# Kernel tuning notes

Hardware: AMD Instinct MI355X
Metric: run time of the kernel (lower is better)

The kernel has to match this reference:

```python
import math
import jax, jax.numpy as jnp
import numpy as np

B, S, D, L = 8, 4096, 1024, 16

def setup_inputs() -> dict:
    key = jax.random.key(0)
    k1, k2, k3 = jax.random.split(key, 3)
    memory = jax.random.normal(k1, (B, S, D), dtype=jnp.float32)
    summarizer = jax.random.normal(k2, (L, D), dtype=jnp.float32) * 0.02
    w_proj = jax.random.normal(k3, (1, L), dtype=jnp.float32) * (1.0 / math.sqrt(L))
    return {"memory": memory, "summarizer": summarizer, "w_proj": w_proj}

def reference(memory, summarizer, w_proj):
    # scores: [B, L, S] = summarizer @ memory^T / sqrt(D)
    d = summarizer.shape[-1]
    scores = jnp.einsum('ld,bsd->bls', summarizer, memory) / jnp.sqrt(jnp.asarray(d, memory.dtype))
    p_attn = jax.nn.softmax(scores, axis=-1)            # softmax over sequence S
    ctx = jnp.einsum('bls,bsd->bld', p_attn, memory)    # [B, L, D]
    # nn.Linear(L, 1, bias=False) applied to ctx.transpose(-1,-2): [B, D, L] @ W^T -> [B, D, 1]
    out = jnp.einsum('bld,l->bd', ctx, w_proj[0])       # [B, D]
    return out[:, None, :]                              # [B, 1, D] after final transpose
```

## Files before the change

### kernel.cpp

```cpp
#include <hip/hip_runtime.h>

#define SS 4096
#define DD 1024
#define LL 16

typedef __attribute__((ext_vector_type(8))) short short8;
typedef __attribute__((ext_vector_type(4))) float fl4;
typedef __attribute__((ext_vector_type(2))) float fl2;

static __device__ __forceinline__ short f2bf(float f) {
    unsigned u = __float_as_uint(f);
    u += 0x7FFFu + ((u >> 16) & 1u);
    return (short)(u >> 16);
}

static __device__ __forceinline__ short8 pack8(fl4 a, fl4 b) {
    short8 r;
    r[0] = f2bf(a[0]); r[1] = f2bf(a[1]); r[2] = f2bf(a[2]); r[3] = f2bf(a[3]);
    r[4] = f2bf(b[0]); r[5] = f2bf(b[1]); r[6] = f2bf(b[2]); r[7] = f2bf(b[3]);
    return r;
}

__global__ __launch_bounds__(512) void k_main(const float* __restrict__ mem,
                                              const float* __restrict__ summ,
                                              float* __restrict__ part,
                                              float* __restrict__ Zpart) {
    __shared__ float scr[2][8][256];
    __shared__ float e_lds[2][16][LL];

    int blk = blockIdx.x;
    int b   = blk >> 6;
    int s0  = (blk & 63) << 6;
    int t    = threadIdx.x;
    int wv   = t >> 6;
    int lane = t & 63;
    int o  = lane & 15;
    int qd = lane >> 4;

    short8 afr[4];
    {
        const float* arow = summ + o * DD + wv * 128 + qd * 8;
        #pragma unroll
        for (int j = 0; j < 4; ++j) {
            fl4 a0 = *(const fl4*)(arow + j * 32);
            fl4 a1 = *(const fl4*)(arow + j * 32 + 4);
            afr[j] = pack8(a0, a1);
        }
    }

    fl2 ctx[LL];
    #pragma unroll
    for (int l = 0; l < LL; ++l) ctx[l] = (fl2){0.f, 0.f};
    fl4 zacc = {0.f, 0.f, 0.f, 0.f};
    const float scale = 0.03125f;

    const float* gb = mem + ((size_t)b * SS + s0) * DD;

    #pragma unroll 2
    for (int c = 0; c < 4; ++c) {
        const float* brow = gb + (size_t)(c * 16 + o) * DD + wv * 128 + qd * 8;
        fl4 acc = {0.f, 0.f, 0.f, 0.f};
        #pragma unroll
        for (int j = 0; j < 4; ++j) {
            fl4 f0 = *(const fl4*)(brow + j * 32);
            fl4 f1 = *(const fl4*)(brow + j * 32 + 4);
            acc = __builtin_amdgcn_mfma_f32_16x16x32_bf16(afr[j], pack8(f0, f1),
                                                          acc, 0, 0, 0);
        }
        *(fl4*)&scr[c & 1][wv][lane * 4] = acc;
        asm volatile("s_waitcnt lgkmcnt(0)" ::: "memory");
        __builtin_amdgcn_s_barrier();
        __builtin_amdgcn_sched_barrier(0);

        if (wv == 0) {
            fl4 sum = {0.f, 0.f, 0.f, 0.f};
            #pragma unroll
            for (int w8 = 0; w8 < 8; ++w8)
                sum += *(const fl4*)&scr[c & 1][w8][lane * 4];
            fl4 ev;
            #pragma unroll
            for (int r = 0; r < 4; ++r) ev[r] = __expf(sum[r] * scale);
            *(fl4*)&e_lds[c & 1][o][qd * 4] = ev;
            zacc += ev;
        }
        asm volatile("s_waitcnt lgkmcnt(0)" ::: "memory");
        __builtin_amdgcn_s_barrier();
        __builtin_amdgcn_sched_barrier(0);

        const float* mrow = gb + (size_t)(c * 16) * DD + wv * 128 + lane * 2;
        #pragma unroll 4
        for (int s = 0; s < 16; ++s) {
            fl2 m2 = *(const fl2*)(mrow + (size_t)s * DD);
            #pragma unroll
            for (int g4 = 0; g4 < 4; ++g4) {
                fl4 e4 = *(const fl4*)&e_lds[c & 1][s][g4 * 4];
                ctx[g4 * 4 + 0] += e4[0] * m2;
                ctx[g4 * 4 + 1] += e4[1] * m2;
                ctx[g4 * 4 + 2] += e4[2] * m2;
                ctx[g4 * 4 + 3] += e4[3] * m2;
            }
        }
    }

    float* pp = part + (size_t)blk * LL * DD + wv * 128 + lane * 2;
    #pragma unroll
    for (int l = 0; l < LL; ++l) *(fl2*)(pp + (size_t)l * DD) = ctx[l];

    if (wv == 0) {
        #pragma unroll
        for (int r = 0; r < 4; ++r) {
            float v = zacc[r];
            v += __shfl_xor(v, 1, 64);
            v += __shfl_xor(v, 2, 64);
            v += __shfl_xor(v, 4, 64);
            v += __shfl_xor(v, 8, 64);
            zacc[r] = v;
        }
        if (o == 0) *(fl4*)&Zpart[blk * LL + qd * 4] = zacc;
    }
}

__global__ __launch_bounds__(256) void k_out(const float* __restrict__ part,
                                             const float* __restrict__ Zpart,
                                             const float* __restrict__ w,
                                             float* __restrict__ out) {
    int blkid = blockIdx.x;
    int b  = blkid >> 5;
    int d0 = (blkid & 31) << 5;
    int t = threadIdx.x;
    __shared__ float coef[LL];
    __shared__ fl4 red[32][8];

    if (t < LL) {
        float Z = 0.f;
        #pragma unroll
        for (int s = 0; s < 64; ++s) Z += Zpart[(b * 64 + s) * LL + t];
        coef[t] = w[t] / Z;
    }
    __syncthreads();

    int dq = t & 7;
    int sg = t >> 3;
    fl4 acc = {0.f, 0.f, 0.f, 0.f};
    #pragma unroll
    for (int h = 0; h < 2; ++h) {
        const float* pb = part + (size_t)(b * 64 + sg + h * 32) * LL * DD + d0 + dq * 4;
        #pragma unroll
        for (int l = 0; l < LL; ++l) {
            fl4 v = *(const fl4*)(pb + (size_t)l * DD);
            acc += coef[l] * v;
        }
    }
    red[sg][dq] = acc;
    __syncthreads();

    if (t < 8) {
        fl4 s = {0.f, 0.f, 0.f, 0.f};
        #pragma unroll
        for (int g = 0; g < 32; ++g) s += red[g][t];
        *(fl4*)&out[b * DD + d0 + t * 4] = s;
    }
}

extern "C" void kernel_launch(void* const* d_in, const int* in_sizes, int n_in,
                              void* d_out, int out_size, void* d_ws, size_t ws_size,
                              hipStream_t stream) {
    const float* mem  = (const float*)d_in[0];
    const float* summ = (const float*)d_in[1];
    const float* w    = (const float*)d_in[2];
    float* out = (float*)d_out;

    char* ws = (char*)d_ws;
    float* Zpart = (float*)ws;
    float* part  = (float*)(ws + 64 * 1024);

    k_main<<<512, 512, 0, stream>>>(mem, summ, part, Zpart);
    k_out<<<256, 256, 0, stream>>>(part, Zpart, w, out);
}
```

Baseline: 216.6 us.

## Compute full-D scores per wave to remove per-chunk cross-wave reductions

Result: slower. 221.7 us (+2.3%).

```diff
diff --git a/kernel.cpp b/kernel.cpp
--- a/kernel.cpp
+++ b/kernel.cpp
@@ -25,8 +25,9 @@
                                               const float* __restrict__ summ,
                                               float* __restrict__ part,
                                               float* __restrict__ Zpart) {
-    __shared__ float scr[2][8][256];
-    __shared__ float e_lds[2][16][LL];
+    __shared__ short8 a_lds[32][64];
+    __shared__ float  e_lds[64][LL];
+    __shared__ float  z_lds[8][LL];
 
     int blk = blockIdx.x;
     int b   = blk >> 6;
@@ -37,86 +38,80 @@
     int o  = lane & 15;
     int qd = lane >> 4;
 
-    short8 afr[4];
+    #pragma unroll
+    for (int p = 0; p < 4; ++p) {
+        int j = p * 8 + wv;
+        const float* ar = summ + o * DD + j * 32 + qd * 8;
+        fl4 x0 = *(const fl4*)ar;
+        fl4 x1 = *(const fl4*)(ar + 4);
+        a_lds[j][lane] = pack8(x0, x1);
+    }
+    __syncthreads();
+
+    const float* gb = mem + ((size_t)b * SS + s0) * DD;
+    const float scale = 0.03125f;
+
+    fl4 acc = {0.f, 0.f, 0.f, 0.f};
     {
-        const float* arow = summ + o * DD + wv * 128 + qd * 8;
+        const float* brow = gb + (size_t)(wv * 8 + (o & 7)) * DD + qd * 8;
         #pragma unroll
-        for (int j = 0; j < 4; ++j) {
-            fl4 a0 = *(const fl4*)(arow + j * 32);
-            fl4 a1 = *(const fl4*)(arow + j * 32 + 4);
-            afr[j] = pack8(a0, a1);
+        for (int j = 0; j < 32; ++j) {
+            fl4 f0 = *(const fl4*)(brow + j * 32);
+            fl4 f1 = *(const fl4*)(brow + j * 32 + 4);
+            short8 af = a_lds[j][lane];
+            acc = __builtin_amdgcn_mfma_f32_16x16x32_bf16(af, pack8(f0, f1),
+                                                          acc, 0, 0, 0);
         }
     }
+
+    fl4 ev;
+    #pragma unroll
+    for (int r = 0; r < 4; ++r) ev[r] = __expf(acc[r] * scale);
+
+    fl4 zv = ev;
+    #pragma unroll
+    for (int r = 0; r < 4; ++r) {
+        float v = zv[r];
+        v += __shfl_xor(v, 1, 64);
+        v += __shfl_xor(v, 2, 64);
+        v += __shfl_xor(v, 4, 64);
+        zv[r] = v;
+    }
+    if (o == 0) *(fl4*)&z_lds[wv][qd * 4] = zv;
+    if (o < 8)  *(fl4*)&e_lds[wv * 8 + o][qd * 4] = ev;
+
+    asm volatile("s_waitcnt lgkmcnt(0)" ::: "memory");
+    __builtin_amdgcn_s_barrier();
+    __builtin_amdgcn_sched_barrier(0);
 
     fl2 ctx[LL];
     #pragma unroll
     for (int l = 0; l < LL; ++l) ctx[l] = (fl2){0.f, 0.f};
-    fl4 zacc = {0.f, 0.f, 0.f, 0.f};
-    const float scale = 0.03125f;
 
-    const float* gb = mem + ((size_t)b * SS + s0) * DD;
-
-    #pragma unroll 2
-    for (int c = 0; c < 4; ++c) {
-        const float* brow = gb + (size_t)(c * 16 + o) * DD + wv * 128 + qd * 8;
-        fl4 acc = {0.f, 0.f, 0.f, 0.f};
+    const float* mrow = gb + t * 2;
+    #pragma unroll 8
+    for (int s = 0; s < 64; ++s) {
+        fl2 m2 = *(const fl2*)(mrow + (size_t)s * DD);
+        const fl4* er = (const fl4*)&e_lds[s][0];
+        fl4 e0 = er[0], e1 = er[1], e2 = er[2], e3 = er[3];
         #pragma unroll
         for (int j = 0; j < 4; ++j) {
-            fl4 f0 = *(const fl4*)(brow + j * 32);
-            fl4 f1 = *(const fl4*)(brow + j * 32 + 4);
-            acc = __builtin_amdgcn_mfma_f32_16x16x32_bf16(afr[j], pack8(f0, f1),
-                                                          acc, 0, 0, 0);
-        }
-        *(fl4*)&scr[c & 1][wv][lane * 4] = acc;
-        asm volatile("s_waitcnt lgkmcnt(0)" ::: "memory");
-        __builtin_amdgcn_s_barrier();
-        __builtin_amdgcn_sched_barrier(0);
-
-        if (wv == 0) {
-            fl4 sum = {0.f, 0.f, 0.f, 0.f};
-            #pragma unroll
-            for (int w8 = 0; w8 < 8; ++w8)
-                sum += *(const fl4*)&scr[c & 1][w8][lane * 4];
-            fl4 ev;
-            #pragma unroll
-            for (int r = 0; r < 4; ++r) ev[r] = __expf(sum[r] * scale);
-            *(fl4*)&e_lds[c & 1][o][qd * 4] = ev;
-            zacc += ev;
-        }
-        asm volatile("s_waitcnt lgkmcnt(0)" ::: "memory");
-        __builtin_amdgcn_s_barrier();
-        __builtin_amdgcn_sched_barrier(0);
-
-        const float* mrow = gb + (size_t)(c * 16) * DD + wv * 128 + lane * 2;
-        #pragma unroll 4
-        for (int s = 0; s < 16; ++s) {
-            fl2 m2 = *(const fl2*)(mrow + (size_t)s * DD);
-            #pragma unroll
-            for (int g4 = 0; g4 < 4; ++g4) {
-                fl4 e4 = *(const fl4*)&e_lds[c & 1][s][g4 * 4];
-                ctx[g4 * 4 + 0] += e4[0] * m2;
-                ctx[g4 * 4 + 1] += e4[1] * m2;
-                ctx[g4 * 4 + 2] += e4[2] * m2;
-                ctx[g4 * 4 + 3] += e4[3] * m2;
-            }
+            ctx[j]      += e0[j] * m2;
+            ctx[4 + j]  += e1[j] * m2;
+            ctx[8 + j]  += e2[j] * m2;
+            ctx[12 + j] += e3[j] * m2;
         }
     }
 
-    float* pp = part + (size_t)blk * LL * DD + wv * 128 + lane * 2;
+    float* pp = part + (size_t)blk * LL * DD + t * 2;
     #pragma unroll
     for (int l = 0; l < LL; ++l) *(fl2*)(pp + (size_t)l * DD) = ctx[l];
 
-    if (wv == 0) {
+    if (t < LL) {
+        float Z = 0.f;
         #pragma unroll
-        for (int r = 0; r < 4; ++r) {
-            float v = zacc[r];
-            v += __shfl_xor(v, 1, 64);
-            v += __shfl_xor(v, 2, 64);
-            v += __shfl_xor(v, 4, 64);
-            v += __shfl_xor(v, 8, 64);
-            zacc[r] = v;
-        }
-        if (o == 0) *(fl4*)&Zpart[blk * LL + qd * 4] = zacc;
+        for (int w8 = 0; w8 < 8; ++w8) Z += z_lds[w8][t];
+        Zpart[blk * LL + t] = Z;
     }
 }
 
```
